# Optimization experiments

Hardware: AMD Instinct MI355X
Metric: run time of the kernel (lower is better)

The kernel has to match this reference:

```python
import jax, jax.numpy as jnp
import numpy as np

B, S, C, HD = 2, 4096, 2048, 128
H = C // HD  # 16 heads
EPS = 1.1920929e-07  # torch RMSNorm default eps for float32 (finfo.eps)


def _make_rope(seq_len, head_dim):
    # Standard RoPE 2x2 rotation matrices: [1, S, 1, head_dim//2, 2, 2]
    half = head_dim // 2
    freqs = 1.0 / (10000.0 ** (np.arange(0, half, dtype=np.float32) / half))
    ang = np.arange(seq_len, dtype=np.float32)[:, None] * freqs[None, :]  # [S, half]
    cos, sin = np.cos(ang), np.sin(ang)
    rot = np.stack([np.stack([cos, -sin], axis=-1),
                    np.stack([sin, cos], axis=-1)], axis=-2)  # [S, half, 2, 2]
    return jnp.asarray(rot[None, :, None])  # [1, S, 1, half, 2, 2]


def setup_inputs() -> dict:
    key = jax.random.key(0)
    ks = jax.random.split(key, 9)
    sc = 1.0 / np.sqrt(C)
    return {
        "x": jax.random.normal(ks[0], (B, S, C), jnp.float32),
        "rope": _make_rope(S, HD),
        "wq": jax.random.normal(ks[1], (C, C), jnp.float32) * sc,
        "bq": jax.random.normal(ks[2], (C,), jnp.float32) * 0.01,
        "wk": jax.random.normal(ks[3], (C, C), jnp.float32) * sc,
        "bk": jax.random.normal(ks[4], (C,), jnp.float32) * 0.01,
        "wv": jax.random.normal(ks[5], (C, C), jnp.float32) * sc,
        "bv": jax.random.normal(ks[6], (C,), jnp.float32) * 0.01,
        "q_norm_w": jnp.ones((HD,), jnp.float32),
        "k_norm_w": jnp.ones((HD,), jnp.float32),
    }


def _rmsnorm(t, w):
    t32 = t.astype(jnp.float32)
    inv = jax.lax.rsqrt(jnp.mean(t32 * t32, axis=-1, keepdims=True) + EPS)
    return (t32 * inv * w).astype(t.dtype)


def _apply_rotary(t, rope):
    # t: [B, S, H, HD] -> pairs [B, S, H, HD//2, 1, 2]; rope: [1, S, 1, HD//2, 2, 2]
    t32 = t.reshape(*t.shape[:-1], HD // 2, 1, 2).astype(jnp.float32)
    out = (rope * t32).sum(axis=-1)  # [B, S, H, HD//2, 2]
    return out.reshape(t.shape).astype(t.dtype)


def reference(x, rope, wq, bq, wk, bk, wv, bv, q_norm_w, k_norm_w):
    # QKV projections (torch Linear: x @ W^T + b)
    q = (jnp.einsum('bsc,oc->bso', x, wq) + bq).reshape(B, S, H, HD)
    k = (jnp.einsum('bsc,oc->bso', x, wk) + bk).reshape(B, S, H, HD)
    v = (jnp.einsum('bsc,oc->bso', x, wv) + bv).reshape(B, S, H, HD)
    # Per-head RMSNorm on q, k (in float32, cast back), then rotary
    q = _apply_rotary(_rmsnorm(q, q_norm_w), rope)
    k = _apply_rotary(_rmsnorm(k, k_norm_w), rope)
    return (q, k, v)
```

## Files before the change

### kernel.cpp

```cpp
#include <hip/hip_runtime.h>


#define M_DIM 8192
#define N_DIM 6144
#define K_DIM 2048
#define NKT 32
#define EPS_RMS 1.1920929e-07f

typedef __bf16 bf16x8 __attribute__((ext_vector_type(8)));
typedef float f32x4 __attribute__((ext_vector_type(4)));

__device__ __forceinline__ void gload16(const void* g, void* l) {
  __builtin_amdgcn_global_load_lds(
      (const __attribute__((address_space(1))) unsigned int*)g,
      (__attribute__((address_space(3))) unsigned int*)l, 16, 0, 0);
}

__device__ __forceinline__ unsigned ldsoff(const void* p) {
  return (unsigned)(unsigned long long)(const __attribute__((address_space(3))) char*)p;
}

__device__ __forceinline__ unsigned short f2bf(float f) {
  union { float f; unsigned u; } x; x.f = f;
  unsigned r = x.u + 0x7FFFu + ((x.u >> 16) & 1u);
  return (unsigned short)(r >> 16);
}

__global__ void __launch_bounds__(256) cvt_kernel(const float* __restrict__ s,
                                                  unsigned short* __restrict__ d, int n4) {
  int i = blockIdx.x * blockDim.x + threadIdx.x;
  const int stride = gridDim.x * blockDim.x;
  for (; i < n4; i += stride) {
    const float4 v = reinterpret_cast<const float4*>(s)[i];
    ushort4 o;
    o.x = f2bf(v.x); o.y = f2bf(v.y); o.z = f2bf(v.z); o.w = f2bf(v.w);
    reinterpret_cast<ushort4*>(d)[i] = o;
  }
}

#define DSR(dst, base, IMM) \
  asm volatile("ds_read_b128 %0, %1 offset:" IMM : "=v"(dst) : "v"(base))

#define MFMA_PH(MH, NH)                                                              \
  {                                                                                  \
    _Pragma("unroll")                                                                \
    for (int mf4 = 0; mf4 < 4; ++mf4) {                                              \
      _Pragma("unroll")                                                              \
      for (int nf2 = 0; nf2 < 2; ++nf2) {                                            \
        f32x4& c = acc[(MH) * 4 + mf4][(NH) * 2 + nf2];                              \
        c = __builtin_amdgcn_mfma_f32_16x16x32_bf16(                                 \
            __builtin_bit_cast(bf16x8, Af[mf4][0]),                                  \
            __builtin_bit_cast(bf16x8, Bf[nf2][0]), c, 0, 0, 0);                     \
        c = __builtin_amdgcn_mfma_f32_16x16x32_bf16(                                 \
            __builtin_bit_cast(bf16x8, Af[mf4][1]),                                  \
            __builtin_bit_cast(bf16x8, Bf[nf2][1]), c, 0, 0, 0);                     \
      }                                                                              \
    }                                                                                \
  }

__global__ void __launch_bounds__(512, 2) gemm_fused(
    const unsigned short* __restrict__ xbf, const unsigned short* __restrict__ wbf,
    const float* __restrict__ rope,
    const float* __restrict__ bq, const float* __restrict__ bk, const float* __restrict__ bv,
    const float* __restrict__ qnw, const float* __restrict__ knw,
    float* __restrict__ dout) {
  const int id = blockIdx.x;
  const int sw = (id & 7) * 96 + (id >> 3);
  const int bm = sw / 24;
  const int bn = sw - bm * 24;
  const int m0 = bm << 8, n0 = bn << 8;
  const int tid = threadIdx.x;
  const int w = tid >> 6, l = tid & 63;
  const int l15 = l & 15, lhi = l >> 4;
  const int wr = w >> 2, wc = w & 3;

  __shared__ __align__(16) unsigned short As[32768];
  __shared__ __align__(16) unsigned short Bs[32768];

  const int srow = tid >> 3;
  const int schunk = (tid & 7) ^ (srow & 7);
  const unsigned short* aSrc = xbf + ((size_t)(m0 + srow) << 11) + (schunk << 3);
  const unsigned short* bSrc = wbf + ((size_t)(n0 + srow) << 11) + (schunk << 3);
  char* aDst = (char*)As + (w << 10);
  char* bDst = (char*)Bs + (w << 10);

#define STA(KT, Q) gload16(aSrc + ((Q) << 17) + ((KT) << 6), aDst + ((((KT) & 1) << 15) + ((Q) << 13)))
#define STB(KT, Q) gload16(bSrc + ((Q) << 17) + ((KT) << 6), bDst + ((((KT) & 1) << 15) + ((Q) << 13)))

  const int sl0 = ((lhi ^ (l15 & 7)) << 4);
  const int sl1 = (((lhi + 4) ^ (l15 & 7)) << 4);
  unsigned a0 = ldsoff(As) + (wr << 14) + (l15 << 7) + sl0;
  unsigned a1 = ldsoff(As) + (wr << 14) + (l15 << 7) + sl1;
  unsigned b0 = ldsoff(Bs) + (wc << 13) + (l15 << 7) + sl0;
  unsigned b1 = ldsoff(Bs) + (wc << 13) + (l15 << 7) + sl1;

  f32x4 acc[8][4];
#pragma unroll
  for (int i = 0; i < 8; ++i)
#pragma unroll
    for (int j = 0; j < 4; ++j) acc[i][j] = (f32x4){0.f, 0.f, 0.f, 0.f};

  f32x4 Af[4][2], Bf[2][2];

  STA(0, 0); STA(0, 1); STA(0, 2); STA(0, 3);
  STB(0, 0); STB(0, 1); STB(0, 2); STB(0, 3);
  STA(1, 0); STA(1, 2);
  STA(1, 1); STA(1, 3); STB(1, 0); STB(1, 1); STB(1, 2); STB(1, 3);
  asm volatile("s_waitcnt vmcnt(8)");
  __builtin_amdgcn_s_barrier();

  for (int kt = 0; kt < NKT; ++kt) {
    DSR(Af[0][0], a0, "0");    DSR(Af[1][0], a0, "2048");
    DSR(Af[2][0], a0, "4096"); DSR(Af[3][0], a0, "6144");
    DSR(Af[0][1], a1, "0");    DSR(Af[1][1], a1, "2048");
    DSR(Af[2][1], a1, "4096"); DSR(Af[3][1], a1, "6144");
    DSR(Bf[0][0], b0, "0");    DSR(Bf[1][0], b0, "2048");
    DSR(Bf[0][1], b1, "0");    DSR(Bf[1][1], b1, "2048");
    if (kt >= 1 && kt <= NKT - 2) {
      STA(kt + 1, 1); STA(kt + 1, 3);
      STB(kt + 1, 0); STB(kt + 1, 1); STB(kt + 1, 2); STB(kt + 1, 3);
    }
    __builtin_amdgcn_s_barrier();
    asm volatile("s_waitcnt lgkmcnt(0)");
    __builtin_amdgcn_sched_barrier(0);
    __builtin_amdgcn_s_setprio(1);
    MFMA_PH(0, 0);
    __builtin_amdgcn_s_setprio(0);
    __builtin_amdgcn_s_barrier();
    DSR(Bf[0][0], b0, "4096"); DSR(Bf[1][0], b0, "6144");
    DSR(Bf[0][1], b1, "4096"); DSR(Bf[1][1], b1, "6144");
    __builtin_amdgcn_s_barrier();
    asm volatile("s_waitcnt lgkmcnt(0)");
    __builtin_amdgcn_sched_barrier(0);
    __builtin_amdgcn_s_setprio(1);
    MFMA_PH(0, 1);
    __builtin_amdgcn_s_setprio(0);
    __builtin_amdgcn_s_barrier();
    DSR(Af[0][0], a0, "8192");  DSR(Af[1][0], a0, "10240");
    DSR(Af[2][0], a0, "12288"); DSR(Af[3][0], a0, "14336");
    DSR(Af[0][1], a1, "8192");  DSR(Af[1][1], a1, "10240");
    DSR(Af[2][1], a1, "12288"); DSR(Af[3][1], a1, "14336");
    __builtin_amdgcn_s_barrier();
    asm volatile("s_waitcnt lgkmcnt(0)");
    __builtin_amdgcn_sched_barrier(0);
    __builtin_amdgcn_s_setprio(1);
    MFMA_PH(1, 1);
    __builtin_amdgcn_s_setprio(0);
    __builtin_amdgcn_s_barrier();
    DSR(Bf[0][0], b0, "0"); DSR(Bf[1][0], b0, "2048");
    DSR(Bf[0][1], b1, "0"); DSR(Bf[1][1], b1, "2048");
    if (kt <= NKT - 3) { STA(kt + 2, 0); STA(kt + 2, 2); }
    __builtin_amdgcn_s_barrier();
    asm volatile("s_waitcnt lgkmcnt(0)");
    __builtin_amdgcn_sched_barrier(0);
    __builtin_amdgcn_s_setprio(1);
    MFMA_PH(1, 0);
    __builtin_amdgcn_s_setprio(0);
    if (kt < NKT - 2)       { asm volatile("s_waitcnt vmcnt(2)"); }
    else if (kt == NKT - 2) { asm volatile("s_waitcnt vmcnt(0)"); }
    __builtin_amdgcn_s_barrier();
    a0 ^= 32768u; a1 ^= 32768u; b0 ^= 32768u; b1 ^= 32768u;
  }

  __syncthreads();
  float* scr = (float*)As;
  const int sec = bn >> 3;
  const int nsec = (n0 & 2047) + (wc << 6);
  const float* bias = sec == 0 ? bq : (sec == 1 ? bk : bv);
  float biasv[4];
#pragma unroll
  for (int nf = 0; nf < 4; ++nf) biasv[nf] = bias[nsec + nf * 16 + l15];
  const size_t outBase = ((size_t)sec << 24);

  if (sec < 2) {
    const float* nwp = sec ? knw : qnw;
    const int colh = (wc & 1) << 6;
    float nwv[4];
#pragma unroll
    for (int nf = 0; nf < 4; ++nf) nwv[nf] = nwp[colh + nf * 16 + l15];
    float ssv[8][4];
#pragma unroll
    for (int mf = 0; mf < 8; ++mf) {
#pragma unroll
      for (int j = 0; j < 4; ++j) {
        float ss = 0.f;
#pragma unroll
        for (int nf = 0; nf < 4; ++nf) {
          const float t = acc[mf][nf][j] + biasv[nf];
          ss += t * t;
        }
        ss += __shfl_xor(ss, 1);
        ss += __shfl_xor(ss, 2);
        ss += __shfl_xor(ss, 4);
        ss += __shfl_xor(ss, 8);
        ssv[mf][j] = ss;
      }
    }
    if (l15 == 0) {
#pragma unroll
      for (int mf = 0; mf < 8; ++mf)
#pragma unroll
        for (int j = 0; j < 4; ++j)
          scr[(w << 7) + mf * 16 + (lhi << 2) + j] = ssv[mf][j];
    }
    __syncthreads();
#pragma unroll
    for (int mf = 0; mf < 8; ++mf) {
#pragma unroll
      for (int j = 0; j < 4; ++j) {
        const float tot = ssv[mf][j] + scr[((w ^ 1) << 7) + mf * 16 + (lhi << 2) + j];
        const float inv = rsqrtf(tot * (1.0f / 128.0f) + EPS_RMS);
        const int m = m0 + (wr << 7) + mf * 16 + (lhi << 2) + j;
        const float* rp = rope + ((size_t)(m & 4095) << 8);
        float* orow = dout + outBase + ((size_t)m << 11) + nsec + l15;
#pragma unroll
        for (int nf = 0; nf < 4; ++nf) {
          const float tn = (acc[mf][nf][j] + biasv[nf]) * inv * nwv[nf];
          const float pn = __shfl_xor(tn, 1);
          const int ch = colh + nf * 16 + l15;
          const int jr = ch >> 1;
          const float o = fmaf(rp[jr << 2], tn, rp[(jr << 2) + 1 + (ch & 1)] * pn);
          orow[nf << 4] = o;
        }
      }
    }
  } else {
#pragma unroll
    for (int mf = 0; mf < 8; ++mf)
#pragma unroll
      for (int j = 0; j < 4; ++j) {
        const int m = m0 + (wr << 7) + mf * 16 + (lhi << 2) + j;
        float* orow = dout + outBase + ((size_t)m << 11) + nsec + l15;
#pragma unroll
        for (int nf = 0; nf < 4; ++nf) orow[nf << 4] = acc[mf][nf][j] + biasv[nf];
      }
  }
}

extern "C" void kernel_launch(void* const* d_in, const int* in_sizes, int n_in,
                              void* d_out, int out_size, void* d_ws, size_t ws_size,
                              hipStream_t stream) {
  const float* x = (const float*)d_in[0];
  const float* rope = (const float*)d_in[1];
  const float* wq = (const float*)d_in[2];
  const float* bq = (const float*)d_in[3];
  const float* wk = (const float*)d_in[4];
  const float* bk = (const float*)d_in[5];
  const float* wv = (const float*)d_in[6];
  const float* bv = (const float*)d_in[7];
  const float* qnw = (const float*)d_in[8];
  const float* knw = (const float*)d_in[9];

  unsigned short* xbf = (unsigned short*)d_ws;
  unsigned short* wbf = xbf + (size_t)M_DIM * K_DIM;

  cvt_kernel<<<2048, 256, 0, stream>>>(x, xbf, M_DIM * K_DIM / 4);
  cvt_kernel<<<1024, 256, 0, stream>>>(wq, wbf, K_DIM * K_DIM / 4);
  cvt_kernel<<<1024, 256, 0, stream>>>(wk, wbf + (size_t)K_DIM * K_DIM, K_DIM * K_DIM / 4);
  cvt_kernel<<<1024, 256, 0, stream>>>(wv, wbf + (size_t)2 * K_DIM * K_DIM, K_DIM * K_DIM / 4);

  gemm_fused<<<(M_DIM / 256) * (N_DIM / 256), 512, 0, stream>>>(
      xbf, wbf, rope, bq, bk, bv, qnw, knw, (float*)d_out);
}
```

Before: 287.1 us.

## Keep both B fragment halves in registers and reschedule GEMM prefetch pipeline

Bf is extended to hold both N-halves of the B fragment, so the fourth MFMA phase reuses already-loaded registers and one LDS reread plus its barrier pair is dropped. The global-to-LDS prefetch now covers a single k-tile instead of two, spread across phases with new vmcnt waits, and the trailing __syncthreads before the epilogue is removed. Together this cuts LDS traffic and barriers per iteration at the cost of more VGPRs and less prefetch depth, which may expose global load latency. Removing the final sync depends on the last loop barrier to make reuse of LDS as scratch safe.

```diff
diff --git a/kernel.cpp b/kernel.cpp
--- a/kernel.cpp
+++ b/kernel.cpp
@@ -50,10 +50,10 @@
         f32x4& c = acc[(MH) * 4 + mf4][(NH) * 2 + nf2];                              \
         c = __builtin_amdgcn_mfma_f32_16x16x32_bf16(                                 \
             __builtin_bit_cast(bf16x8, Af[mf4][0]),                                  \
-            __builtin_bit_cast(bf16x8, Bf[nf2][0]), c, 0, 0, 0);                     \
+            __builtin_bit_cast(bf16x8, Bf[NH][nf2][0]), c, 0, 0, 0);                 \
         c = __builtin_amdgcn_mfma_f32_16x16x32_bf16(                                 \
             __builtin_bit_cast(bf16x8, Af[mf4][1]),                                  \
-            __builtin_bit_cast(bf16x8, Bf[nf2][1]), c, 0, 0, 0);                     \
+            __builtin_bit_cast(bf16x8, Bf[NH][nf2][1]), c, 0, 0, 0);                 \
       }                                                                              \
     }                                                                                \
   }
@@ -84,8 +84,8 @@
   char* aDst = (char*)As + (w << 10);
   char* bDst = (char*)Bs + (w << 10);
 
-#define STA(KT, Q) gload16(aSrc + ((Q) << 17) + ((KT) << 6), aDst + ((((KT) & 1) << 15) + ((Q) << 13)))
-#define STB(KT, Q) gload16(bSrc + ((Q) << 17) + ((KT) << 6), bDst + ((((KT) & 1) << 15) + ((Q) << 13)))
+#define STA(KT, Q) gload16(aSrc + ((size_t)(Q) << 17) + ((KT) << 6), aDst + ((((KT) & 1) << 15) + ((Q) << 13)))
+#define STB(KT, Q) gload16(bSrc + ((size_t)(Q) << 17) + ((KT) << 6), bDst + ((((KT) & 1) << 15) + ((Q) << 13)))
 
   const int sl0 = ((lhi ^ (l15 & 7)) << 4);
   const int sl1 = (((lhi + 4) ^ (l15 & 7)) << 4);
@@ -100,26 +100,24 @@
 #pragma unroll
     for (int j = 0; j < 4; ++j) acc[i][j] = (f32x4){0.f, 0.f, 0.f, 0.f};
 
-  f32x4 Af[4][2], Bf[2][2];
-
-  STA(0, 0); STA(0, 1); STA(0, 2); STA(0, 3);
+  f32x4 Af[4][2];
+  f32x4 Bf[2][2][2];
+
+  STA(0, 0); STA(0, 2);
   STB(0, 0); STB(0, 1); STB(0, 2); STB(0, 3);
-  STA(1, 0); STA(1, 2);
-  STA(1, 1); STA(1, 3); STB(1, 0); STB(1, 1); STB(1, 2); STB(1, 3);
-  asm volatile("s_waitcnt vmcnt(8)");
+  STA(0, 1); STA(0, 3);
+  asm volatile("s_waitcnt vmcnt(2)");
   __builtin_amdgcn_s_barrier();
 
   for (int kt = 0; kt < NKT; ++kt) {
+    const bool notLast = (kt < NKT - 1);
     DSR(Af[0][0], a0, "0");    DSR(Af[1][0], a0, "2048");
     DSR(Af[2][0], a0, "4096"); DSR(Af[3][0], a0, "6144");
     DSR(Af[0][1], a1, "0");    DSR(Af[1][1], a1, "2048");
     DSR(Af[2][1], a1, "4096"); DSR(Af[3][1], a1, "6144");
-    DSR(Bf[0][0], b0, "0");    DSR(Bf[1][0], b0, "2048");
-    DSR(Bf[0][1], b1, "0");    DSR(Bf[1][1], b1, "2048");
-    if (kt >= 1 && kt <= NKT - 2) {
-      STA(kt + 1, 1); STA(kt + 1, 3);
-      STB(kt + 1, 0); STB(kt + 1, 1); STB(kt + 1, 2); STB(kt + 1, 3);
-    }
+    DSR(Bf[0][0][0], b0, "0");    DSR(Bf[0][1][0], b0, "2048");
+    DSR(Bf[0][0][1], b1, "0");    DSR(Bf[0][1][1], b1, "2048");
+    if (notLast) { STA(kt + 1, 0); STA(kt + 1, 2); STB(kt + 1, 0); STB(kt + 1, 1); }
     __builtin_amdgcn_s_barrier();
     asm volatile("s_waitcnt lgkmcnt(0)");
     __builtin_amdgcn_sched_barrier(0);
@@ -127,42 +125,35 @@
     MFMA_PH(0, 0);
     __builtin_amdgcn_s_setprio(0);
     __builtin_amdgcn_s_barrier();
-    DSR(Bf[0][0], b0, "4096"); DSR(Bf[1][0], b0, "6144");
-    DSR(Bf[0][1], b1, "4096"); DSR(Bf[1][1], b1, "6144");
+    DSR(Bf[1][0][0], b0, "4096"); DSR(Bf[1][1][0], b0, "6144");
+    DSR(Bf[1][0][1], b1, "4096"); DSR(Bf[1][1][1], b1, "6144");
+    if (notLast) { STB(kt + 1, 2); STB(kt + 1, 3); }
     __builtin_amdgcn_s_barrier();
     asm volatile("s_waitcnt lgkmcnt(0)");
     __builtin_amdgcn_sched_barrier(0);
     __builtin_amdgcn_s_setprio(1);
     MFMA_PH(0, 1);
     __builtin_amdgcn_s_setprio(0);
+    if (notLast) { asm volatile("s_waitcnt vmcnt(6)"); }
+    else         { asm volatile("s_waitcnt vmcnt(0)"); }
     __builtin_amdgcn_s_barrier();
     DSR(Af[0][0], a0, "8192");  DSR(Af[1][0], a0, "10240");
     DSR(Af[2][0], a0, "12288"); DSR(Af[3][0], a0, "14336");
     DSR(Af[0][1], a1, "8192");  DSR(Af[1][1], a1, "10240");
     DSR(Af[2][1], a1, "12288"); DSR(Af[3][1], a1, "14336");
+    if (notLast) { STA(kt + 1, 1); STA(kt + 1, 3); }
     __builtin_amdgcn_s_barrier();
     asm volatile("s_waitcnt lgkmcnt(0)");
     __builtin_amdgcn_sched_barrier(0);
     __builtin_amdgcn_s_setprio(1);
     MFMA_PH(1, 1);
-    __builtin_amdgcn_s_setprio(0);
-    __builtin_amdgcn_s_barrier();
-    DSR(Bf[0][0], b0, "0"); DSR(Bf[1][0], b0, "2048");
-    DSR(Bf[0][1], b1, "0"); DSR(Bf[1][1], b1, "2048");
-    if (kt <= NKT - 3) { STA(kt + 2, 0); STA(kt + 2, 2); }
-    __builtin_amdgcn_s_barrier();
-    asm volatile("s_waitcnt lgkmcnt(0)");
-    __builtin_amdgcn_sched_barrier(0);
-    __builtin_amdgcn_s_setprio(1);
     MFMA_PH(1, 0);
     __builtin_amdgcn_s_setprio(0);
-    if (kt < NKT - 2)       { asm volatile("s_waitcnt vmcnt(2)"); }
-    else if (kt == NKT - 2) { asm volatile("s_waitcnt vmcnt(0)"); }
+    if (notLast) { asm volatile("s_waitcnt vmcnt(2)"); }
     __builtin_amdgcn_s_barrier();
     a0 ^= 32768u; a1 ^= 32768u; b0 ^= 32768u; b1 ^= 32768u;
   }
 
-  __syncthreads();
   float* scr = (float*)As;
   const int sec = bn >> 3;
   const int nsec = (n0 & 2047) + (wc << 6);
```

Result: faster. 265.2 us (-7.6%).
